# Kernel tuning notes

Hardware: AMD Instinct MI355X
Metric: run time of the kernel (lower is better)

The kernel has to match this reference:

```python
import jax, jax.numpy as jnp
import numpy as np

B, T, D = 1, 2048, 1024
E, DFF = 8, 4096


def setup_inputs() -> dict:
    key = jax.random.key(0)
    k1, k2, k3, k4 = jax.random.split(key, 4)
    x = jax.random.normal(k1, (B, T, D), dtype=jnp.float32)
    Wg = jax.random.normal(k2, (D, E), dtype=jnp.float32) * (1.0 / np.sqrt(D))
    w1 = jax.random.normal(k3, (D, DFF), dtype=jnp.float32) * (1.0 / np.sqrt(D))
    w2 = jax.random.normal(k4, (DFF, D), dtype=jnp.float32) * (1.0 / np.sqrt(DFF))
    return {"x": x, "Wg": Wg, "w1": w1, "w2": w2}


def _gating(logits):
    # logits: [S, E]; capacity = S (per source code)
    S, num_e = logits.shape
    gates = jax.nn.softmax(logits.astype(jnp.float32), axis=1)  # [S,E] fp32
    idx1 = jnp.argmax(gates, axis=1)                            # top-1 expert
    mask1 = jax.nn.one_hot(idx1, num_e, dtype=jnp.int32)        # [S,E]
    logits_ex1 = jnp.where(mask1.astype(bool), -jnp.inf, logits)
    idx2 = jnp.argmax(logits_ex1, axis=1)                       # top-2 expert
    mask2 = jax.nn.one_hot(idx2, num_e, dtype=jnp.int32)
    # slot position of each token inside its expert buffer
    loc1 = jnp.cumsum(mask1, axis=0) - 1                        # [S,E]
    loc2 = jnp.cumsum(mask2, axis=0) - 1 + jnp.sum(mask1, axis=0, keepdims=True)
    loc1_s = jnp.sum(loc1 * mask1, axis=1)                      # [S] int
    loc2_s = jnp.sum(loc2 * mask2, axis=1)
    g1 = jnp.sum(gates * mask1, axis=1)                         # [S]
    g2 = jnp.sum(gates * mask2, axis=1)
    denom = jnp.maximum(g1 + g2, jnp.finfo(jnp.float32).eps)
    g1, g2 = g1 / denom, g2 / denom
    cap = S
    loc1_sc = jax.nn.one_hot(loc1_s, cap, dtype=jnp.float32)    # [S,C]
    loc2_sc = jax.nn.one_hot(loc2_s, cap, dtype=jnp.float32)
    # combine_weights: [S,E,C]
    combine = (g1[:, None] * mask1)[:, :, None] * loc1_sc[:, None, :] \
            + (g2[:, None] * mask2)[:, :, None] * loc2_sc[:, None, :]
    dispatch_mask = combine != 0
    return combine.astype(logits.dtype), dispatch_mask


def reference(x, Wg, w1, w2):
    d_model = x.shape[2]
    xs = x.reshape(-1, d_model)                                  # [S,D]
    logits = xs @ Wg                                             # gate linear
    combine, dispatch_mask = _gating(logits)
    # one-hot scatter dispatch: [S,E,C] x [S,D] -> [E,C,D]
    dispatched = jnp.einsum('sec,sm->ecm', dispatch_mask.astype(jnp.float32), xs)
    # all-to-all is an identity permutation of the expert dim in single-process ref
    expert_out = jax.nn.relu(dispatched @ w1) @ w2               # [E,C,D]
    # one-hot gather combine: [S,E,C] x [E,C,D] -> [S,D]
    out = jnp.einsum('sec,ecm->sm', combine, expert_out)
    return out.reshape(x.shape)
```

## Files before the change

### kernel.cpp

```cpp
#include <hip/hip_runtime.h>
#include <stdint.h>


typedef __attribute__((ext_vector_type(4))) float f32x4;
typedef __attribute__((ext_vector_type(16))) float f32x16;
typedef __attribute__((ext_vector_type(8))) short bf16x8;

#define GPTR(p) (const __attribute__((address_space(1))) void*)(p)
#define LPTR(p) (__attribute__((address_space(3))) void*)(p)

__device__ __forceinline__ ushort f2bf(float f) {
  uint32_t u = __float_as_uint(f);
  uint32_t r = (u + 0x7FFFu + ((u >> 16) & 1u)) >> 16;
  return (ushort)r;
}
__device__ __forceinline__ float bf2f(ushort u) {
  return __uint_as_float((uint32_t)u << 16);
}

__device__ __forceinline__ void tile_transpose(const float* __restrict__ in,
                                               ushort* __restrict__ out,
                                               int R, int C, int bx, int by,
                                               int tx, int ty) {
  __shared__ float tile[32][33];
  const int c0 = bx * 32, r0 = by * 32;
#pragma unroll
  for (int i = 0; i < 32; i += 8)
    tile[ty + i][tx] = in[(size_t)(r0 + ty + i) * C + (c0 + tx)];
  __syncthreads();
#pragma unroll
  for (int i = 0; i < 32; i += 8)
    out[(size_t)(c0 + ty + i) * R + (r0 + tx)] = f2bf(tile[tx][ty + i]);
}

__global__ void prep(const float* __restrict__ x, const float* __restrict__ w1,
                     const float* __restrict__ w2, ushort* __restrict__ xb,
                     ushort* __restrict__ w1t, ushort* __restrict__ w2t) {
  const int b = blockIdx.x;
  const int tx = threadIdx.x, ty = threadIdx.y;
  if (b < 2048) {
    int i = b * 256 + ty * 32 + tx;
    float4 v = ((const float4*)x)[i];
    ushort4 o;
    o.x = f2bf(v.x); o.y = f2bf(v.y); o.z = f2bf(v.z); o.w = f2bf(v.w);
    ((ushort4*)xb)[i] = o;
  } else if (b < 6144) {
    int b2 = b - 2048;
    tile_transpose(w1, w1t, 1024, 4096, b2 & 127, b2 >> 7, tx, ty);
  } else {
    int b3 = b - 6144;
    tile_transpose(w2, w2t, 4096, 1024, b3 & 31, b3 >> 5, tx, ty);
  }
}

__global__ void reduce_out(float* __restrict__ out, const ushort* __restrict__ pb,
                           int SD) {
  int i = blockIdx.x * blockDim.x + threadIdx.x;
  if (i >= SD / 4) return;
  f32x4 a = ((const f32x4*)out)[i];
#pragma unroll
  for (int j = 0; j < 3; ++j) {
    ushort4 u = ((const ushort4*)(pb + (size_t)j * SD))[i];
    a[0] += bf2f(u.x); a[1] += bf2f(u.y); a[2] += bf2f(u.z); a[3] += bf2f(u.w);
  }
  ((f32x4*)out)[i] = a;
}

template <int MODE>
__global__ __launch_bounds__(512) void gemm_pipe(const ushort* __restrict__ A,
                                                 const ushort* __restrict__ Bt,
                                                 void* __restrict__ C0,
                                                 void* __restrict__ C1,
                                                 int M, int N, int Ks, int Ktot,
                                                 int ncx, int cpz) {
  constexpr int BM = 128, BN = 256, BK = 64;
  __shared__ ushort As[3][BM * BK];
  __shared__ ushort Bs[3][BN * BK];

  const int tid = threadIdx.x;
  const int lane = tid & 63, wid = tid >> 6;
  const int wr = wid >> 2, wc = wid & 3;

  const int ck = blockIdx.x & 7;
  const int w = blockIdx.x >> 3;
  const int bz = ck / cpz;
  const int rem = ck % cpz;
  const int bx = (rem % ncx) * 4 + (w & 3);
  const int by = (rem / ncx) * 8 + (w >> 2);
  const int row0 = by * BM, col0 = bx * BN;
  const int kbase = bz * Ks;

  f32x16 acc[2][2];
#pragma unroll
  for (int m = 0; m < 2; ++m)
#pragma unroll
    for (int n = 0; n < 2; ++n) acc[m][n] = (f32x16)(0.f);

  const int rA = tid >> 3;
  const int cb = (tid & 7) * 16;
  auto stage_part = [&](int buf, int k0, int p) {
    if (p == 0) {
#pragma unroll
      for (int i = 0; i < 2; ++i) {
        int r = i * 64 + rA;
        int csw = cb ^ ((r & 7) << 4);
        __builtin_amdgcn_global_load_lds(
            GPTR((const char*)(A + (size_t)(row0 + r) * Ktot + k0) + csw),
            LPTR((char*)&As[buf][0] + i * 8192 + wid * 1024), 16, 0, 0);
      }
    } else {
#pragma unroll
      for (int j2 = 0; j2 < 2; ++j2) {
        int j = (p - 1) * 2 + j2;
        int r = j * 64 + rA;
        int csw = cb ^ ((r & 7) << 4);
        __builtin_amdgcn_global_load_lds(
            GPTR((const char*)(Bt + (size_t)(col0 + r) * Ktot + k0) + csw),
            LPTR((char*)&Bs[buf][0] + j * 8192 + wid * 1024), 16, 0, 0);
      }
    }
  };
  auto stage = [&](int buf, int k0) {
    stage_part(buf, k0, 0); stage_part(buf, k0, 1); stage_part(buf, k0, 2);
  };

  const int nt = Ks / BK;
  stage(0, kbase);
  stage(1, kbase + BK);

  for (int t = 0; t < nt; ++t) {
    if (t < nt - 1) asm volatile("s_waitcnt vmcnt(6)" ::: "memory");
    else            asm volatile("s_waitcnt vmcnt(0)" ::: "memory");
    __builtin_amdgcn_sched_barrier(0);
    __builtin_amdgcn_s_barrier();
    __builtin_amdgcn_sched_barrier(0);

    const ushort* Ab = As[t % 3];
    const ushort* Bb = Bs[t % 3];
    const bool pf = (t + 2 < nt);
    const int knext = kbase + (t + 2) * BK;
    const int pbuf = (t + 2) % 3;

    bf16x8 a[2][2], b[2][2];
    auto read_slice = [&](int s, int sb) {
      const int kb2 = s * 32 + (lane >> 5) * 16;
#pragma unroll
      for (int m = 0; m < 2; ++m) {
        int R = wr * 64 + m * 32 + (lane & 31);
        a[sb][m] = *(const bf16x8*)((const char*)Ab + R * 128 + (kb2 ^ ((R & 7) << 4)));
      }
#pragma unroll
      for (int n = 0; n < 2; ++n) {
        int R = wc * 64 + n * 32 + (lane & 31);
        b[sb][n] = *(const bf16x8*)((const char*)Bb + R * 128 + (kb2 ^ ((R & 7) << 4)));
      }
    };

    read_slice(0, 0);
#pragma unroll
    for (int s = 0; s < 4; ++s) {
      if (s < 3) read_slice(s + 1, (s + 1) & 1);
      if (s < 3 && pf) stage_part(pbuf, knext, s);
      __builtin_amdgcn_s_setprio(1);
#pragma unroll
      for (int m = 0; m < 2; ++m)
#pragma unroll
        for (int n = 0; n < 2; ++n)
          acc[m][n] = __builtin_amdgcn_mfma_f32_32x32x16_bf16(a[s & 1][m], b[s & 1][n],
                                                              acc[m][n], 0, 0, 0);
      __builtin_amdgcn_s_setprio(0);
    }
  }

  const int rbase = row0 + wr * 64, cbase = col0 + wc * 64;
#pragma unroll
  for (int m = 0; m < 2; ++m) {
#pragma unroll
    for (int n = 0; n < 2; ++n) {
      const int col = cbase + n * 32 + (lane & 31);
#pragma unroll
      for (int r = 0; r < 16; ++r) {
        const int row = rbase + m * 32 + (r & 3) + 8 * (r >> 2) + 4 * (lane >> 5);
        float v = acc[m][n][r];
        size_t idx = (size_t)row * N + col;
        if (MODE == 1) {
          v = v > 0.f ? v : 0.f;
          ((ushort*)C0)[idx] = f2bf(v);
        } else {
          if (bz == 0)
            ((float*)C0)[idx] = v;
          else
            ((ushort*)C1)[(size_t)(bz - 1) * M * N + idx] = f2bf(v);
        }
      }
    }
  }
}

extern "C" void kernel_launch(void* const* d_in, const int* in_sizes, int n_in,
                              void* d_out, int out_size, void* d_ws, size_t ws_size,
                              hipStream_t stream) {
  const float* x  = (const float*)d_in[0];
  const float* w1 = (const float*)d_in[2];
  const float* w2 = (const float*)d_in[3];
  float* out = (float*)d_out;

  constexpr int S = 2048, D = 1024, F = 4096;
  char* ws = (char*)d_ws;
  ushort* xb  = (ushort*)(ws);
  ushort* w1t = (ushort*)(ws + (size_t)S * D * 2);
  ushort* w2t = (ushort*)(ws + (size_t)(S * D + F * D) * 2);
  ushort* H   = (ushort*)(ws + (size_t)(S * D + 2 * F * D) * 2);
  ushort* pb = (ushort*)(ws);

  hipLaunchKernelGGL(prep, dim3(10240), dim3(32, 8), 0, stream,
                     x, w1, w2, xb, w1t, w2t);
  hipLaunchKernelGGL((gemm_pipe<1>), dim3(256), dim3(512), 0, stream,
                     xb, w1t, (void*)H, nullptr, S, F, D, D, 4, 8);
  hipLaunchKernelGGL((gemm_pipe<2>), dim3(256), dim3(512), 0, stream,
                     H, w2t, (void*)out, (void*)pb, S, D, F / 4, F, 1, 2);
  hipLaunchKernelGGL(reduce_out, dim3((S * D / 4 + 255) / 256), dim3(256), 0, stream,
                     out, pb, S * D);
}
```

Measured before the change: 69.84 us.

## Restructure GEMM main loop into barrier-synced phases and widen weight transpose tiles

The GEMM inner loop now runs two phases per K tile. Each phase loads two LDS slices, issues the next-tile prefetch, and then executes eight MFMAs between workgroup barriers, in a ping-pong style meant to keep waves aligned and overlap memory with compute. The weight-transpose prep kernel switches to 64x64 tiles with float4 loads and ushort4 stores, which cuts the block count and should improve global access efficiency. The risks are extra barriers per tile and LDS bank conflicts in the strided column reads of the new transpose.

```diff
diff --git a/kernel.cpp b/kernel.cpp
--- a/kernel.cpp
+++ b/kernel.cpp
@@ -18,38 +18,50 @@
   return __uint_as_float((uint32_t)u << 16);
 }
 
-__device__ __forceinline__ void tile_transpose(const float* __restrict__ in,
-                                               ushort* __restrict__ out,
-                                               int R, int C, int bx, int by,
-                                               int tx, int ty) {
-  __shared__ float tile[32][33];
-  const int c0 = bx * 32, r0 = by * 32;
-#pragma unroll
-  for (int i = 0; i < 32; i += 8)
-    tile[ty + i][tx] = in[(size_t)(r0 + ty + i) * C + (c0 + tx)];
-  __syncthreads();
-#pragma unroll
-  for (int i = 0; i < 32; i += 8)
-    out[(size_t)(c0 + ty + i) * R + (r0 + tx)] = f2bf(tile[tx][ty + i]);
-}
-
-__global__ void prep(const float* __restrict__ x, const float* __restrict__ w1,
-                     const float* __restrict__ w2, ushort* __restrict__ xb,
-                     ushort* __restrict__ w1t, ushort* __restrict__ w2t) {
-  const int b = blockIdx.x;
-  const int tx = threadIdx.x, ty = threadIdx.y;
+__global__ __launch_bounds__(256) void prep(const float* __restrict__ x,
+                                            const float* __restrict__ w1,
+                                            const float* __restrict__ w2,
+                                            ushort* __restrict__ xb,
+                                            ushort* __restrict__ w1t,
+                                            ushort* __restrict__ w2t) {
+  const int b = blockIdx.x, tid = threadIdx.x;
   if (b < 2048) {
-    int i = b * 256 + ty * 32 + tx;
+    int i = b * 256 + tid;
     float4 v = ((const float4*)x)[i];
     ushort4 o;
     o.x = f2bf(v.x); o.y = f2bf(v.y); o.z = f2bf(v.z); o.w = f2bf(v.w);
     ((ushort4*)xb)[i] = o;
-  } else if (b < 6144) {
-    int b2 = b - 2048;
-    tile_transpose(w1, w1t, 1024, 4096, b2 & 127, b2 >> 7, tx, ty);
-  } else {
-    int b3 = b - 6144;
-    tile_transpose(w2, w2t, 4096, 1024, b3 & 31, b3 >> 5, tx, ty);
+    return;
+  }
+  const float* in;
+  ushort* outp;
+  int R, C, bt;
+  if (b < 3072) { bt = b - 2048; in = w1; outp = w1t; R = 1024; C = 4096; }
+  else          { bt = b - 3072; in = w2; outp = w2t; R = 4096; C = 1024; }
+  const int ntx = C / 64;
+  const int bx = bt % ntx, by = bt / ntx;
+  const int c0 = bx * 64, r0 = by * 64;
+  __shared__ float tile[64][65];
+  const int tx = tid & 15, ty = tid >> 4;
+#pragma unroll
+  for (int rr = 0; rr < 64; rr += 16) {
+    float4 v = *(const float4*)&in[(size_t)(r0 + ty + rr) * C + c0 + tx * 4];
+    tile[ty + rr][tx * 4 + 0] = v.x;
+    tile[ty + rr][tx * 4 + 1] = v.y;
+    tile[ty + rr][tx * 4 + 2] = v.z;
+    tile[ty + rr][tx * 4 + 3] = v.w;
+  }
+  __syncthreads();
+#pragma unroll
+  for (int cc = 0; cc < 64; cc += 16) {
+    const int c = ty + cc;
+    const int r = tx * 4;
+    ushort4 o;
+    o.x = f2bf(tile[r + 0][c]);
+    o.y = f2bf(tile[r + 1][c]);
+    o.z = f2bf(tile[r + 2][c]);
+    o.w = f2bf(tile[r + 3][c]);
+    *(ushort4*)&outp[(size_t)(c0 + c) * R + r0 + r] = o;
   }
 }
 
@@ -120,55 +132,66 @@
       }
     }
   };
-  auto stage = [&](int buf, int k0) {
-    stage_part(buf, k0, 0); stage_part(buf, k0, 1); stage_part(buf, k0, 2);
-  };
 
   const int nt = Ks / BK;
-  stage(0, kbase);
-  stage(1, kbase + BK);
+  stage_part(0, kbase, 0); stage_part(0, kbase, 1); stage_part(0, kbase, 2);
+  stage_part(1, kbase + BK, 0); stage_part(1, kbase + BK, 1); stage_part(1, kbase + BK, 2);
+  asm volatile("s_waitcnt vmcnt(6)" ::: "memory");
+  __builtin_amdgcn_sched_barrier(0);
+  __builtin_amdgcn_s_barrier();
+  __builtin_amdgcn_sched_barrier(0);
 
   for (int t = 0; t < nt; ++t) {
-    if (t < nt - 1) asm volatile("s_waitcnt vmcnt(6)" ::: "memory");
-    else            asm volatile("s_waitcnt vmcnt(0)" ::: "memory");
-    __builtin_amdgcn_sched_barrier(0);
-    __builtin_amdgcn_s_barrier();
-    __builtin_amdgcn_sched_barrier(0);
-
     const ushort* Ab = As[t % 3];
     const ushort* Bb = Bs[t % 3];
     const bool pf = (t + 2 < nt);
     const int knext = kbase + (t + 2) * BK;
     const int pbuf = (t + 2) % 3;
 
-    bf16x8 a[2][2], b[2][2];
-    auto read_slice = [&](int s, int sb) {
-      const int kb2 = s * 32 + (lane >> 5) * 16;
-#pragma unroll
-      for (int m = 0; m < 2; ++m) {
-        int R = wr * 64 + m * 32 + (lane & 31);
-        a[sb][m] = *(const bf16x8*)((const char*)Ab + R * 128 + (kb2 ^ ((R & 7) << 4)));
-      }
-#pragma unroll
-      for (int n = 0; n < 2; ++n) {
-        int R = wc * 64 + n * 32 + (lane & 31);
-        b[sb][n] = *(const bf16x8*)((const char*)Bb + R * 128 + (kb2 ^ ((R & 7) << 4)));
-      }
-    };
-
-    read_slice(0, 0);
-#pragma unroll
-    for (int s = 0; s < 4; ++s) {
-      if (s < 3) read_slice(s + 1, (s + 1) & 1);
-      if (s < 3 && pf) stage_part(pbuf, knext, s);
+#pragma unroll
+    for (int p = 0; p < 2; ++p) {
+      bf16x8 a2[2][2], b2[2][2];
+#pragma unroll
+      for (int sl = 0; sl < 2; ++sl) {
+        const int s = p * 2 + sl;
+        const int kb2 = s * 32 + (lane >> 5) * 16;
+#pragma unroll
+        for (int m = 0; m < 2; ++m) {
+          int R = wr * 64 + m * 32 + (lane & 31);
+          a2[sl][m] = *(const bf16x8*)((const char*)Ab + R * 128 + (kb2 ^ ((R & 7) << 4)));
+        }
+#pragma unroll
+        for (int n = 0; n < 2; ++n) {
+          int R = wc * 64 + n * 32 + (lane & 31);
+          b2[sl][n] = *(const bf16x8*)((const char*)Bb + R * 128 + (kb2 ^ ((R & 7) << 4)));
+        }
+      }
+      if (pf) {
+        if (p == 0) { stage_part(pbuf, knext, 0); stage_part(pbuf, knext, 1); }
+        else        { stage_part(pbuf, knext, 2); }
+      }
+      __builtin_amdgcn_sched_barrier(0);
+      __builtin_amdgcn_s_barrier();
+      asm volatile("s_waitcnt lgkmcnt(0)" ::: "memory");
+      __builtin_amdgcn_sched_barrier(0);
       __builtin_amdgcn_s_setprio(1);
 #pragma unroll
-      for (int m = 0; m < 2; ++m)
-#pragma unroll
-        for (int n = 0; n < 2; ++n)
-          acc[m][n] = __builtin_amdgcn_mfma_f32_32x32x16_bf16(a[s & 1][m], b[s & 1][n],
-                                                              acc[m][n], 0, 0, 0);
+      for (int sl = 0; sl < 2; ++sl)
+#pragma unroll
+        for (int m = 0; m < 2; ++m)
+#pragma unroll
+          for (int n = 0; n < 2; ++n)
+            acc[m][n] = __builtin_amdgcn_mfma_f32_32x32x16_bf16(a2[sl][m], b2[sl][n],
+                                                                acc[m][n], 0, 0, 0);
       __builtin_amdgcn_s_setprio(0);
+      __builtin_amdgcn_sched_barrier(0);
+      if (p == 1 && t < nt - 1) {
+        if (t + 2 < nt) asm volatile("s_waitcnt vmcnt(6)" ::: "memory");
+        else            asm volatile("s_waitcnt vmcnt(0)" ::: "memory");
+        __builtin_amdgcn_sched_barrier(0);
+      }
+      __builtin_amdgcn_s_barrier();
+      __builtin_amdgcn_sched_barrier(0);
     }
   }
 
@@ -213,7 +236,7 @@
   ushort* H   = (ushort*)(ws + (size_t)(S * D + 2 * F * D) * 2);
   ushort* pb = (ushort*)(ws);
 
-  hipLaunchKernelGGL(prep, dim3(10240), dim3(32, 8), 0, stream,
+  hipLaunchKernelGGL(prep, dim3(4096), dim3(256), 0, stream,
                      x, w1, w2, xb, w1t, w2t);
   hipLaunchKernelGGL((gemm_pipe<1>), dim3(256), dim3(512), 0, stream,
                      xb, w1t, (void*)H, nullptr, S, F, D, D, 4, 8);
```

Measured after the change: 70.68 us. Within noise of the previous version (+1.2%).
